# Kernel optimization log

Measured on AMD Instinct MI355X. Metric: run time of the kernel, lower is better.

Reference implementation:

```python
import jax, jax.numpy as jnp
import numpy as np

B, S, D, DFF = 8, 2048, 1024, 4096

def setup_inputs() -> dict:
    key = jax.random.key(0)
    ks = jax.random.split(key, 11)
    s = 0.02
    return {
        "x":  jax.random.normal(ks[0], (B, S, D), dtype=jnp.float32),
        "Wq": jax.random.normal(ks[1], (D, D), dtype=jnp.float32) * s,
        "bq": jnp.zeros((D,), dtype=jnp.float32),
        "Wk": jax.random.normal(ks[2], (D, D), dtype=jnp.float32) * s,
        "bk": jnp.zeros((D,), dtype=jnp.float32),
        "Wv": jax.random.normal(ks[3], (D, D), dtype=jnp.float32) * s,
        "bv": jnp.zeros((D,), dtype=jnp.float32),
        "W1": jax.random.normal(ks[4], (DFF, D), dtype=jnp.float32) * s,
        "b1": jnp.zeros((DFF,), dtype=jnp.float32),
        "W2": jax.random.normal(ks[5], (D, DFF), dtype=jnp.float32) * s,
        "b2": jnp.zeros((D,), dtype=jnp.float32),
    }

def reference(x, Wq, bq, Wk, bk, Wv, bv, W1, b1, W2, b2):
    # qkv projections (torch Linear: x @ W.T + b)
    q = jnp.einsum('bsd,ed->bse', x, Wq) + bq
    k = jnp.einsum('bsd,ed->bse', x, Wk) + bk
    v = jnp.einsum('bsd,ed->bse', x, Wv) + bv
    # single-head scaled dot-product attention with causal mask (decoder=True)
    scale = 1.0 / jnp.sqrt(jnp.asarray(q.shape[-1], q.dtype))
    scores = jnp.einsum('bqd,bkd->bqk', q, k) * scale  # (B,S,S)
    causal = jnp.tril(jnp.ones((scores.shape[-2], scores.shape[-1]), dtype=bool))
    scores = jnp.where(causal, scores, jnp.asarray(-jnp.inf, scores.dtype))
    attn = jax.nn.softmax(scores, axis=-1)
    attn_out = jnp.einsum('bqk,bkd->bqd', attn, v)
    # MLP: linear_2(gelu(linear_1(.)))  — exact (erf) GELU as in torch default
    h = jax.nn.gelu(jnp.einsum('bsd,fd->bsf', attn_out, W1) + b1, approximate=False)
    return jnp.einsum('bsf,df->bsd', h, W2) + b2
```

## Files before the change

kernel.cpp:

```cpp
#include <hip/hip_runtime.h>
#include <hip/hip_bf16.h>

#define NB   8
#define SS   2048
#define DD   1024
#define DFFN 4096
#define MTOT (NB*SS)

typedef unsigned short u16;
typedef __attribute__((ext_vector_type(4))) float f32x4;
typedef __attribute__((ext_vector_type(8))) short bf16x8;
typedef __attribute__((ext_vector_type(4))) int i32x4;
typedef __attribute__((ext_vector_type(4))) unsigned short u16x4;
typedef __attribute__((ext_vector_type(8))) unsigned short u16x8;

__device__ __forceinline__ u16 f2bf(float f) {
  union { float f; unsigned u; } c; c.f = f;
  unsigned r = c.u + 0x7FFFu + ((c.u >> 16) & 1u);
  return (u16)(r >> 16);
}

__device__ __forceinline__ void gload16(const void* g, void* l) {
  __builtin_amdgcn_global_load_lds(
      (const __attribute__((address_space(1))) void*)(unsigned long long)g,
      (__attribute__((address_space(3))) void*)(unsigned)(unsigned long long)l,
      16, 0, 0);
}

__device__ __forceinline__ bf16x8 dsr128(unsigned addr) {
  i32x4 r;
  asm volatile("ds_read_b128 %0, %1" : "=v"(r) : "v"(addr));
  return __builtin_bit_cast(bf16x8, r);
}

template<int EBIAS, int EGELU, int ESCALE, int EROWSCALE, int OUTMODE, int ETRANS, int CSKIP, int CK>
__global__ __launch_bounds__(256, 3)
void gemm128(const u16* __restrict__ A, const u16* __restrict__ B,
             const float* __restrict__ bias, const float* __restrict__ rowscale,
             void* __restrict__ C,
             int K, int lda, int ldb, int ldc, float scale,
             long long sA, long long sB, long long sC, int sRS)
{
  __shared__ __align__(1024) u16 smem[16384];

  const int nwg = gridDim.x * gridDim.y;
  const int orig = blockIdx.y * gridDim.x + blockIdx.x;
  const int q = nwg >> 3, r = nwg & 7;
  const int xcd = orig & 7, pos0 = orig >> 3;
  const int wg = (xcd < r ? xcd * (q + 1) : r * (q + 1) + (xcd - r) * q) + pos0;
  const int bx = wg % gridDim.x, by = wg / gridDim.x;
  const int row0 = by * 128, col0 = bx * 128;
  if (CSKIP && col0 > row0 + 127) return;

  const int z = blockIdx.z;
  A += (size_t)z * sA;
  B += (size_t)z * sB;

  int nkt = K >> 5;
  if (CK) { int lim = (row0 + 128) >> 5; if (lim < nkt) nkt = lim; }

  const int tid  = threadIdx.x;
  const int wid  = tid >> 6;
  const int lane = tid & 63;
  const int wr = wid >> 1, wc = wid & 1;

  const int srow = wid * 16 + (lane >> 2);
  const int sunit = (lane & 3) ^ ((lane >> 3) & 3);
  const char* gA = (const char*)A + ((size_t)(row0 + srow) * lda + sunit * 8) * 2;
  const char* gB = (const char*)B + ((size_t)(col0 + srow) * ldb + sunit * 8) * 2;
  char* lbase = (char*)smem;
  const size_t ldab = (size_t)64 * lda * 2;
  const size_t ldbb = (size_t)64 * ldb * 2;

  #define STG(t2) { char* lb = lbase + ((t2) & 1) * 16384; size_t kb = (size_t)(t2) * 64; \
      gload16(gA + kb,        lb + wid * 1024);                                           \
      gload16(gA + kb + ldab, lb + 4096 + wid * 1024);                                    \
      gload16(gB + kb,        lb + 8192 + wid * 1024);                                    \
      gload16(gB + kb + ldbb, lb + 8192 + 4096 + wid * 1024); }

  const int fr = lane & 15;
  const int ks16 = ((lane >> 4) & 3) * 16;
  const int xm = ((lane >> 1) & 3) << 4;
  const unsigned sbase = (unsigned)(unsigned long long)(void*)smem;

  f32x4 acc[4][4] = {};

  STG(0);
  asm volatile("s_waitcnt vmcnt(0)");
  asm volatile("s_barrier" ::: "memory");

  for (int t = 0; t < nkt; ++t) {
    if (t + 1 < nkt) STG(t + 1);
    const unsigned cb = sbase + (t & 1) * 16384;
    bf16x8 af[4], bf[4];
#pragma unroll
    for (int m = 0; m < 4; ++m)
      af[m] = dsr128(cb + (((wr * 64 + m * 16 + fr) * 64 + ks16) ^ xm));
#pragma unroll
    for (int n = 0; n < 4; ++n)
      bf[n] = dsr128(cb + ((8192 + (wc * 64 + n * 16 + fr) * 64 + ks16) ^ xm));
    asm volatile("s_waitcnt lgkmcnt(0)");
    __builtin_amdgcn_sched_barrier(0);
    __builtin_amdgcn_s_setprio(1);
#pragma unroll
    for (int m = 0; m < 4; ++m)
#pragma unroll
      for (int n = 0; n < 4; ++n)
        acc[m][n] = __builtin_amdgcn_mfma_f32_16x16x32_bf16(af[m], bf[n], acc[m][n], 0, 0, 0);
    __builtin_amdgcn_s_setprio(0);
    asm volatile("s_waitcnt vmcnt(0)");
    asm volatile("s_barrier" ::: "memory");
  }
  #undef STG

  char* sm = (char*)smem;
  const int r4 = (lane >> 4) * 4;

  if (OUTMODE == 1) {
#pragma unroll
    for (int p = 0; p < 2; ++p) {
      if (wc == p) {
#pragma unroll
        for (int n = 0; n < 4; ++n) {
          const int col = col0 + wc * 64 + n * 16 + fr;
          const int pb = (n * 16 + fr) * 4;
          float bia = EBIAS ? bias[col] : 0.0f;
#pragma unroll
          for (int m = 0; m < 4; ++m) {
#pragma unroll
            for (int j = 0; j < 4; ++j) {
              const int line = wr * 64 + m * 16 + r4 + j;
              float xv = acc[m][n][j];
              if (EBIAS)     xv += bia;
              if (ESCALE)    xv *= scale;
              if (EROWSCALE) xv *= rowscale[z * sRS + row0 + line];
              if (EGELU)     xv = 0.5f * xv * (1.0f + erff(xv * 0.70710678118f));
              *(float*)(sm + ((line * 256 + pb) ^ ((line & 7) << 4))) = xv;
            }
          }
        }
      }
      __syncthreads();
      float* Cb = (float*)C + (size_t)z * sC;
#pragma unroll
      for (int i = 0; i < 8; ++i) {
        const int o = i * 4096 + tid * 16;
        const int line = o >> 8, ps = o & 255;
        f32x4 v = *(const f32x4*)(sm + ((line * 256 + ps) ^ ((line & 7) << 4)));
        *(f32x4*)((char*)(Cb + (size_t)(row0 + line) * ldc + col0 + p * 64) + ps) = v;
      }
      __syncthreads();
    }
  } else if (ETRANS) {
#pragma unroll
    for (int n = 0; n < 4; ++n) {
      const int col = col0 + wc * 64 + n * 16 + fr;
      const int line = wc * 64 + n * 16 + fr;
      float bia = EBIAS ? bias[col] : 0.0f;
#pragma unroll
      for (int m = 0; m < 4; ++m) {
        const int rb = wr * 64 + m * 16 + r4;
        u16x4 pk;
#pragma unroll
        for (int j = 0; j < 4; ++j) {
          float xv = acc[m][n][j];
          if (EBIAS) xv += bia;
          pk[j] = f2bf(xv);
        }
        *(u16x4*)(sm + ((line * 256 + rb * 2) ^ ((line & 7) << 4))) = pk;
      }
    }
    __syncthreads();
    u16* Cb = (u16*)C + (size_t)(row0 >> 11) * (DD * SS) + (row0 & (SS - 1));
#pragma unroll
    for (int i = 0; i < 8; ++i) {
      const int o = i * 4096 + tid * 16;
      const int line = o >> 8, ps = o & 255;
      f32x4 v = *(const f32x4*)(sm + ((line * 256 + ps) ^ ((line & 7) << 4)));
      *(f32x4*)((char*)(Cb + (size_t)(col0 + line) * SS) + ps) = v;
    }
  } else {
#pragma unroll
    for (int n = 0; n < 4; ++n) {
      const int col = col0 + wc * 64 + n * 16 + fr;
      const int pc = (wc * 64 + n * 16 + fr) * 2;
      float bia = EBIAS ? bias[col] : 0.0f;
#pragma unroll
      for (int m = 0; m < 4; ++m) {
#pragma unroll
        for (int j = 0; j < 4; ++j) {
          const int line = wr * 64 + m * 16 + r4 + j;
          float xv = acc[m][n][j];
          if (EBIAS)     xv += bia;
          if (ESCALE)    xv *= scale;
          if (EROWSCALE) xv *= rowscale[z * sRS + row0 + line];
          if (EGELU)     xv = 0.5f * xv * (1.0f + erff(xv * 0.70710678118f));
          u16 u;
          if (OUTMODE == 2) { union { u16 s; _Float16 h; } cu; cu.h = (_Float16)xv; u = cu.s; }
          else u = f2bf(xv);
          *(u16*)(sm + ((line * 256 + pc) ^ ((line & 7) << 4))) = u;
        }
      }
    }
    __syncthreads();
    u16* Cb = (u16*)C + (size_t)z * sC + col0;
#pragma unroll
    for (int i = 0; i < 8; ++i) {
      const int o = i * 4096 + tid * 16;
      const int line = o >> 8, ps = o & 255;
      f32x4 v = *(const f32x4*)(sm + ((line * 256 + ps) ^ ((line & 7) << 4)));
      *(f32x4*)((char*)(Cb + (size_t)(row0 + line) * ldc) + ps) = v;
    }
  }
}

__global__ __launch_bounds__(256) void cvt_bf16_k(const float* __restrict__ in, u16* __restrict__ out, int n4) {
  int i = blockIdx.x * blockDim.x + threadIdx.x;
  if (i < n4) {
    float4 v = ((const float4*)in)[i];
    u16x4 o;
    o.x = f2bf(v.x); o.y = f2bf(v.y); o.z = f2bf(v.z); o.w = f2bf(v.w);
    ((u16x4*)out)[i] = o;
  }
}

__global__ __launch_bounds__(256) void softmax_k(u16* __restrict__ sc, float* __restrict__ rinv, int rows0) {
  const int widx = blockIdx.x * 4 + (threadIdx.x >> 6);
  const int lane = threadIdx.x & 63;
  u16* row = sc + (size_t)widx * SS;
  const int L = (widx & (SS - 1)) + 1;
  float mx = -1e30f;
  for (int k = 0; k < 4; ++k) {
    const int j0 = k * 512 + lane * 8;
    if (j0 < L) {
      u16x8 v = *(const u16x8*)(row + j0);
      int lim = L - j0; if (lim > 8) lim = 8;
#pragma unroll
      for (int e = 0; e < 8; ++e) {
        if (e < lim) { union { u16 u; _Float16 h; } c; c.u = v[e]; mx = fmaxf(mx, (float)c.h); }
      }
    }
  }
#pragma unroll
  for (int o = 32; o >= 1; o >>= 1) mx = fmaxf(mx, __shfl_xor(mx, o));
  float s = 0.0f;
  for (int k = 0; k < 4; ++k) {
    const int j0 = k * 512 + lane * 8;
    u16x8 v = *(const u16x8*)(row + j0);
    u16x8 w;
#pragma unroll
    for (int e = 0; e < 8; ++e) {
      const int j = j0 + e;
      float ev = 0.0f;
      if (j < L) { union { u16 u; _Float16 h; } c; c.u = v[e]; ev = __expf((float)c.h - mx); s += ev; }
      w[e] = f2bf(ev);
    }
    *(u16x8*)(row + j0) = w;
  }
#pragma unroll
  for (int o = 32; o >= 1; o >>= 1) s += __shfl_xor(s, o);
  if (lane == 0) rinv[rows0 + widx] = 1.0f / s;
}

extern "C" void kernel_launch(void* const* d_in, const int* in_sizes, int n_in,
                              void* d_out, int out_size, void* d_ws, size_t ws_size,
                              hipStream_t stream) {
  const float* x  = (const float*)d_in[0];
  const float* Wq = (const float*)d_in[1];
  const float* bq = (const float*)d_in[2];
  const float* Wk = (const float*)d_in[3];
  const float* bk = (const float*)d_in[4];
  const float* Wv = (const float*)d_in[5];
  const float* bv = (const float*)d_in[6];
  const float* W1 = (const float*)d_in[7];
  const float* b1 = (const float*)d_in[8];
  const float* W2 = (const float*)d_in[9];
  const float* b2 = (const float*)d_in[10];

  char* ws = (char*)d_ws;
  u16*  xb   = (u16*)(ws);
  u16*  Wqb  = (u16*)(ws + 33554432);
  u16*  Wkb  = (u16*)(ws + 35651584);
  u16*  Wvb  = (u16*)(ws + 37748736);
  u16*  W1b  = (u16*)(ws + 39845888);
  u16*  W2b  = (u16*)(ws + 48234496);
  u16*  Qb   = (u16*)(ws + 56623104);
  u16*  Kb   = (u16*)(ws + 90177536);
  u16*  Vtb  = (u16*)(ws + 123731968);
  float* rinv = (float*)(ws + 157286400);
  u16*  big  = (u16*)(ws + 157351936);
  u16*  att  = xb;

  const size_t base = 157351936ull;
  const size_t avail = ws_size > base ? ws_size - base : 0;
  int GB = 8; while (GB > 1 && (size_t)GB * 8388608ull > avail) GB >>= 1;
  int MC = 8192; while (MC > 2048 && (size_t)MC * 8192ull > avail) MC >>= 1;

  cvt_bf16_k<<<MTOT * DD / 4 / 256, 256, 0, stream>>>(x, xb, MTOT * DD / 4);
  cvt_bf16_k<<<DD * DD / 4 / 256, 256, 0, stream>>>(Wq, Wqb, DD * DD / 4);
  cvt_bf16_k<<<DD * DD / 4 / 256, 256, 0, stream>>>(Wk, Wkb, DD * DD / 4);
  cvt_bf16_k<<<DD * DD / 4 / 256, 256, 0, stream>>>(Wv, Wvb, DD * DD / 4);
  cvt_bf16_k<<<DFFN * DD / 4 / 256, 256, 0, stream>>>(W1, W1b, DFFN * DD / 4);
  cvt_bf16_k<<<DFFN * DD / 4 / 256, 256, 0, stream>>>(W2, W2b, DFFN * DD / 4);

  gemm128<1,0,0,0,0,0,0,0><<<dim3(DD/128, MTOT/128), 256, 0, stream>>>(
      xb, Wqb, bq, nullptr, (void*)Qb, DD, DD, DD, DD, 0.f, 0, 0, 0, 0);
  gemm128<1,0,0,0,0,0,0,0><<<dim3(DD/128, MTOT/128), 256, 0, stream>>>(
      xb, Wkb, bk, nullptr, (void*)Kb, DD, DD, DD, DD, 0.f, 0, 0, 0, 0);
  gemm128<1,0,0,0,0,1,0,0><<<dim3(DD/128, MTOT/128), 256, 0, stream>>>(
      xb, Wvb, bv, nullptr, (void*)Vtb, DD, DD, DD, DD, 0.f, 0, 0, 0, 0);

  for (int b0 = 0; b0 < NB; b0 += GB) {
    gemm128<0,0,1,0,2,0,1,0><<<dim3(SS/128, SS/128, GB), 256, 0, stream>>>(
        Qb + (size_t)b0 * SS * DD, Kb + (size_t)b0 * SS * DD, nullptr, nullptr,
        (void*)big, DD, DD, DD, SS, 0.03125f,
        (long long)SS * DD, (long long)SS * DD, (long long)SS * SS, 0);
    softmax_k<<<GB * SS / 4, 256, 0, stream>>>(big, rinv, b0 * SS);
    gemm128<0,0,0,1,0,0,0,1><<<dim3(DD/128, SS/128, GB), 256, 0, stream>>>(
        big, Vtb + (size_t)b0 * DD * SS, nullptr, rinv + (size_t)b0 * SS,
        (void*)(att + (size_t)b0 * SS * DD), SS, SS, SS, DD, 0.f,
        (long long)SS * SS, (long long)DD * SS, (long long)SS * DD, SS);
  }

  for (int c = 0; c < MTOT / MC; ++c) {
    u16* h = big;
    gemm128<1,1,0,0,0,0,0,0><<<dim3(DFFN/128, MC/128), 256, 0, stream>>>(
        att + (size_t)c * MC * DD, W1b, b1, nullptr, (void*)h,
        DD, DD, DD, DFFN, 0.f, 0, 0, 0, 0);
    gemm128<1,0,0,0,1,0,0,0><<<dim3(DD/128, MC/128), 256, 0, stream>>>(
        h, W2b, b2, nullptr, (void*)((float*)d_out + (size_t)c * MC * DD),
        DFFN, DFFN, DFFN, DD, 0.f, 0, 0, 0, 0);
  }
}
```

Before: 715.4 us.

## Triple-buffer GEMM LDS staging with two-tile prefetch depth

```diff
diff --git a/kernel.cpp b/kernel.cpp
--- a/kernel.cpp
+++ b/kernel.cpp
@@ -34,14 +34,14 @@
 }
 
 template<int EBIAS, int EGELU, int ESCALE, int EROWSCALE, int OUTMODE, int ETRANS, int CSKIP, int CK>
-__global__ __launch_bounds__(256, 3)
+__global__ __launch_bounds__(256, 4)
 void gemm128(const u16* __restrict__ A, const u16* __restrict__ B,
              const float* __restrict__ bias, const float* __restrict__ rowscale,
              void* __restrict__ C,
              int K, int lda, int ldb, int ldc, float scale,
              long long sA, long long sB, long long sC, int sRS)
 {
-  __shared__ __align__(1024) u16 smem[16384];
+  __shared__ __align__(1024) u16 smem[24576];
 
   const int nwg = gridDim.x * gridDim.y;
   const int orig = blockIdx.y * gridDim.x + blockIdx.x;
@@ -68,14 +68,13 @@
   const int sunit = (lane & 3) ^ ((lane >> 3) & 3);
   const char* gA = (const char*)A + ((size_t)(row0 + srow) * lda + sunit * 8) * 2;
   const char* gB = (const char*)B + ((size_t)(col0 + srow) * ldb + sunit * 8) * 2;
-  char* lbase = (char*)smem;
   const size_t ldab = (size_t)64 * lda * 2;
   const size_t ldbb = (size_t)64 * ldb * 2;
 
-  #define STG(t2) { char* lb = lbase + ((t2) & 1) * 16384; size_t kb = (size_t)(t2) * 64; \
-      gload16(gA + kb,        lb + wid * 1024);                                           \
-      gload16(gA + kb + ldab, lb + 4096 + wid * 1024);                                    \
-      gload16(gB + kb,        lb + 8192 + wid * 1024);                                    \
+  #define STG(t2, bo) { char* lb = (char*)smem + (bo); size_t kb = (size_t)(t2) * 64; \
+      gload16(gA + kb,        lb + wid * 1024);                                       \
+      gload16(gA + kb + ldab, lb + 4096 + wid * 1024);                                \
+      gload16(gB + kb,        lb + 8192 + wid * 1024);                                \
       gload16(gB + kb + ldbb, lb + 8192 + 4096 + wid * 1024); }
 
   const int fr = lane & 15;
@@ -85,32 +84,42 @@
 
   f32x4 acc[4][4] = {};
 
-  STG(0);
-  asm volatile("s_waitcnt vmcnt(0)");
+  STG(0, 0); STG(1, 16384);
+  asm volatile("s_waitcnt vmcnt(4)");
   asm volatile("s_barrier" ::: "memory");
 
-  for (int t = 0; t < nkt; ++t) {
-    if (t + 1 < nkt) STG(t + 1);
-    const unsigned cb = sbase + (t & 1) * 16384;
-    bf16x8 af[4], bf[4];
-#pragma unroll
-    for (int m = 0; m < 4; ++m)
-      af[m] = dsr128(cb + (((wr * 64 + m * 16 + fr) * 64 + ks16) ^ xm));
-#pragma unroll
-    for (int n = 0; n < 4; ++n)
-      bf[n] = dsr128(cb + ((8192 + (wc * 64 + n * 16 + fr) * 64 + ks16) ^ xm));
-    asm volatile("s_waitcnt lgkmcnt(0)");
-    __builtin_amdgcn_sched_barrier(0);
-    __builtin_amdgcn_s_setprio(1);
-#pragma unroll
-    for (int m = 0; m < 4; ++m)
-#pragma unroll
-      for (int n = 0; n < 4; ++n)
-        acc[m][n] = __builtin_amdgcn_mfma_f32_16x16x32_bf16(af[m], bf[n], acc[m][n], 0, 0, 0);
-    __builtin_amdgcn_s_setprio(0);
-    asm volatile("s_waitcnt vmcnt(0)");
-    asm volatile("s_barrier" ::: "memory");
-  }
+  unsigned cb = sbase;
+  unsigned sb = sbase + 32768;
+
+  #define KSTEP_BODY(WAITN)                                                   \
+    bf16x8 af[4], bf[4];                                                      \
+    _Pragma("unroll") for (int m = 0; m < 4; ++m)                             \
+      af[m] = dsr128(cb + (((wr * 64 + m * 16 + fr) * 64 + ks16) ^ xm));      \
+    _Pragma("unroll") for (int n = 0; n < 4; ++n)                             \
+      bf[n] = dsr128(cb + ((8192 + (wc * 64 + n * 16 + fr) * 64 + ks16) ^ xm));\
+    asm volatile("s_waitcnt lgkmcnt(0)");                                     \
+    __builtin_amdgcn_sched_barrier(0);                                        \
+    __builtin_amdgcn_s_setprio(1);                                            \
+    _Pragma("unroll") for (int m = 0; m < 4; ++m)                             \
+      _Pragma("unroll") for (int n = 0; n < 4; ++n)                           \
+        acc[m][n] = __builtin_amdgcn_mfma_f32_16x16x32_bf16(af[m], bf[n], acc[m][n], 0, 0, 0); \
+    __builtin_amdgcn_s_setprio(0);                                            \
+    asm volatile("s_waitcnt vmcnt(" #WAITN ")");                              \
+    asm volatile("s_barrier" ::: "memory");                                   \
+    cb += 16384; if (cb == sbase + 49152) cb = sbase;                         \
+    sb += 16384; if (sb == sbase + 49152) sb = sbase;
+
+  for (int t = 0; t < nkt - 2; ++t) {
+    STG(t + 2, sb - sbase);
+    KSTEP_BODY(4)
+  }
+  {
+    KSTEP_BODY(0)
+  }
+  {
+    KSTEP_BODY(0)
+  }
+  #undef KSTEP_BODY
   #undef STG
 
   char* sm = (char*)smem;
```

New measurement: 724.5 us. Within noise of the previous version (+1.3%).

## Load B fragments directly to registers, triple-buffer A in LDS, fuse QKV GEMMs

Applied to the files above, without the earlier changes.

```diff
diff --git a/kernel.cpp b/kernel.cpp
--- a/kernel.cpp
+++ b/kernel.cpp
@@ -32,12 +32,18 @@
   asm volatile("ds_read_b128 %0, %1" : "=v"(r) : "v"(addr));
   return __builtin_bit_cast(bf16x8, r);
 }
-
-template<int EBIAS, int EGELU, int ESCALE, int EROWSCALE, int OUTMODE, int ETRANS, int CSKIP, int CK>
+__device__ __forceinline__ void gload_b128(bf16x8* d, const char* a) {
+  i32x4 r;
+  asm volatile("global_load_dwordx4 %0, %1, off" : "=v"(r) : "v"(a));
+  *d = __builtin_bit_cast(bf16x8, r);
+}
+
+template<int EBIAS, int EGELU, int ESCALE, int EROWSCALE, int OUTMODE, int CSKIP, int CK>
 __global__ __launch_bounds__(256, 3)
 void gemm128(const u16* __restrict__ A, const u16* __restrict__ B,
-             const float* __restrict__ bias, const float* __restrict__ rowscale,
-             void* __restrict__ C,
+             const float* __restrict__ bias0, const float* __restrict__ bias1,
+             const float* __restrict__ bias2, const float* __restrict__ rowscale,
+             void* __restrict__ C0, void* __restrict__ C1, void* __restrict__ C2,
              int K, int lda, int ldb, int ldc, float scale,
              long long sA, long long sB, long long sC, int sRS)
 {
@@ -63,58 +69,116 @@
   const int wid  = tid >> 6;
   const int lane = tid & 63;
   const int wr = wid >> 1, wc = wid & 1;
-
-  const int srow = wid * 16 + (lane >> 2);
-  const int sunit = (lane & 3) ^ ((lane >> 3) & 3);
-  const char* gA = (const char*)A + ((size_t)(row0 + srow) * lda + sunit * 8) * 2;
-  const char* gB = (const char*)B + ((size_t)(col0 + srow) * ldb + sunit * 8) * 2;
-  char* lbase = (char*)smem;
-  const size_t ldab = (size_t)64 * lda * 2;
-  const size_t ldbb = (size_t)64 * ldb * 2;
-
-  #define STG(t2) { char* lb = lbase + ((t2) & 1) * 16384; size_t kb = (size_t)(t2) * 64; \
-      gload16(gA + kb,        lb + wid * 1024);                                           \
-      gload16(gA + kb + ldab, lb + 4096 + wid * 1024);                                    \
-      gload16(gB + kb,        lb + 8192 + wid * 1024);                                    \
-      gload16(gB + kb + ldbb, lb + 8192 + 4096 + wid * 1024); }
-
   const int fr = lane & 15;
   const int ks16 = ((lane >> 4) & 3) * 16;
   const int xm = ((lane >> 1) & 3) << 4;
+
+  const int sunit = (lane & 3) ^ ((lane >> 3) & 3);
+  const char* gA = (const char*)A +
+      ((size_t)(row0 + wid * 32 + (lane >> 2)) * lda + sunit * 8) * 2;
+  const size_t ldab = (size_t)16 * lda * 2;
   const unsigned sbase = (unsigned)(unsigned long long)(void*)smem;
 
+  const char* gB0 = (const char*)B +
+      ((size_t)(col0 + wc * 64 + fr) * ldb + (lane >> 4) * 8) * 2;
+  const size_t nstep = (size_t)16 * ldb * 2;
+  const char* gB1 = gB0 + nstep;
+  const char* gB2 = gB1 + nstep;
+  const char* gB3 = gB2 + nstep;
+
   f32x4 acc[4][4] = {};
-
-  STG(0);
-  asm volatile("s_waitcnt vmcnt(0)");
+  bf16x8 b0[4], b1[4];
+  unsigned cbo = 0, sbo = 16384;
+  size_t kbo = 128;
+
+  gload_b128(&b0[0], gB0); gload_b128(&b0[1], gB1);
+  gload_b128(&b0[2], gB2); gload_b128(&b0[3], gB3);
+  gB0 += 64; gB1 += 64; gB2 += 64; gB3 += 64;
+  gload16(gA,        (char*)smem + wid * 2048);
+  gload16(gA + ldab, (char*)smem + wid * 2048 + 1024);
+  gload16(gA + 64,        (char*)smem + 8192 + wid * 2048);
+  gload16(gA + 64 + ldab, (char*)smem + 8192 + wid * 2048 + 1024);
+  asm volatile("s_waitcnt vmcnt(2)" ::: "memory");
   asm volatile("s_barrier" ::: "memory");
-
-  for (int t = 0; t < nkt; ++t) {
-    if (t + 1 < nkt) STG(t + 1);
-    const unsigned cb = sbase + (t & 1) * 16384;
-    bf16x8 af[4], bf[4];
+  __builtin_amdgcn_sched_barrier(0);
+
+  #define STEP_MAIN(BC, BN)                                                   \
+  {                                                                           \
+    gload_b128(&BN[0], gB0); gload_b128(&BN[1], gB1);                         \
+    gload_b128(&BN[2], gB2); gload_b128(&BN[3], gB3);                         \
+    gB0 += 64; gB1 += 64; gB2 += 64; gB3 += 64;                               \
+    { char* lb = (char*)smem + sbo + wid * 2048;                              \
+      gload16(gA + kbo,        lb);                                           \
+      gload16(gA + kbo + ldab, lb + 1024); }                                  \
+    kbo += 64;                                                                \
+    bf16x8 af[4];                                                             \
+    _Pragma("unroll") for (int m = 0; m < 4; ++m)                             \
+      af[m] = dsr128(sbase + cbo + (((wr * 64 + m * 16 + fr) * 64 + ks16) ^ xm)); \
+    asm volatile("s_waitcnt lgkmcnt(0)" ::: "memory");                        \
+    __builtin_amdgcn_sched_barrier(0);                                        \
+    __builtin_amdgcn_s_setprio(1);                                            \
+    _Pragma("unroll") for (int m = 0; m < 4; ++m)                             \
+      _Pragma("unroll") for (int n = 0; n < 4; ++n)                           \
+        acc[m][n] = __builtin_amdgcn_mfma_f32_16x16x32_bf16(af[m], BC[n], acc[m][n], 0, 0, 0); \
+    __builtin_amdgcn_s_setprio(0);                                            \
+    __builtin_amdgcn_sched_barrier(0);                                        \
+    asm volatile("s_waitcnt vmcnt(2)" ::: "memory");                          \
+    asm volatile("s_barrier" ::: "memory");                                   \
+    __builtin_amdgcn_sched_barrier(0);                                        \
+    cbo += 8192; if (cbo == 24576) cbo = 0;                                   \
+    sbo += 8192; if (sbo == 24576) sbo = 0;                                   \
+  }
+
+  for (int it = (nkt - 2) >> 1; it > 0; --it) {
+    STEP_MAIN(b0, b1)
+    STEP_MAIN(b1, b0)
+  }
+  #undef STEP_MAIN
+
+  {
+    gload_b128(&b1[0], gB0); gload_b128(&b1[1], gB1);
+    gload_b128(&b1[2], gB2); gload_b128(&b1[3], gB3);
+    bf16x8 af[4];
 #pragma unroll
     for (int m = 0; m < 4; ++m)
-      af[m] = dsr128(cb + (((wr * 64 + m * 16 + fr) * 64 + ks16) ^ xm));
-#pragma unroll
-    for (int n = 0; n < 4; ++n)
-      bf[n] = dsr128(cb + ((8192 + (wc * 64 + n * 16 + fr) * 64 + ks16) ^ xm));
-    asm volatile("s_waitcnt lgkmcnt(0)");
+      af[m] = dsr128(sbase + cbo + (((wr * 64 + m * 16 + fr) * 64 + ks16) ^ xm));
+    asm volatile("s_waitcnt lgkmcnt(0)" ::: "memory");
     __builtin_amdgcn_sched_barrier(0);
     __builtin_amdgcn_s_setprio(1);
 #pragma unroll
     for (int m = 0; m < 4; ++m)
 #pragma unroll
       for (int n = 0; n < 4; ++n)
-        acc[m][n] = __builtin_amdgcn_mfma_f32_16x16x32_bf16(af[m], bf[n], acc[m][n], 0, 0, 0);
+        acc[m][n] = __builtin_amdgcn_mfma_f32_16x16x32_bf16(af[m], b0[n], acc[m][n], 0, 0, 0);
     __builtin_amdgcn_s_setprio(0);
-    asm volatile("s_waitcnt vmcnt(0)");
+    __builtin_amdgcn_sched_barrier(0);
+    asm volatile("s_waitcnt vmcnt(0)" ::: "memory");
     asm volatile("s_barrier" ::: "memory");
-  }
-  #undef STG
+    __builtin_amdgcn_sched_barrier(0);
+    cbo += 8192; if (cbo == 24576) cbo = 0;
+  }
+  {
+    bf16x8 af[4];
+#pragma unroll
+    for (int m = 0; m < 4; ++m)
+      af[m] = dsr128(sbase + cbo + (((wr * 64 + m * 16 + fr) * 64 + ks16) ^ xm));
+    asm volatile("s_waitcnt lgkmcnt(0)" ::: "memory");
+    __builtin_amdgcn_sched_barrier(0);
+#pragma unroll
+    for (int m = 0; m < 4; ++m)
+#pragma unroll
+      for (int n = 0; n < 4; ++n)
+        acc[m][n] = __builtin_amdgcn_mfma_f32_16x16x32_bf16(af[m], b1[n], acc[m][n], 0, 0, 0);
+    asm volatile("s_barrier" ::: "memory");
+    __builtin_amdgcn_sched_barrier(0);
+  }
 
   char* sm = (char*)smem;
   const int r4 = (lane >> 4) * 4;
+  const int sel  = (OUTMODE == 3) ? (col0 >> 10) : 0;
+  const int oc0  = (OUTMODE == 3) ? (col0 & 1023) : col0;
+  const float* bias = (OUTMODE == 3) ? (sel == 0 ? bias0 : sel == 1 ? bias1 : bias2)
+                                     : bias0;
 
   if (OUTMODE == 1) {
 #pragma unroll
@@ -122,7 +186,7 @@
       if (wc == p) {
 #pragma unroll
         for (int n = 0; n < 4; ++n) {
-          const int col = col0 + wc * 64 + n * 16 + fr;
+          const int col = oc0 + wc * 64 + n * 16 + fr;
           const int pb = (n * 16 + fr) * 4;
           float bia = EBIAS ? bias[col] : 0.0f;
 #pragma unroll
@@ -141,48 +205,43 @@
         }
       }
       __syncthreads();
-      float* Cb = (float*)C + (size_t)z * sC;
+      float* Cb = (float*)C0 + (size_t)z * sC;
 #pragma unroll
       for (int i = 0; i < 8; ++i) {
         const int o = i * 4096 + tid * 16;
         const int line = o >> 8, ps = o & 255;
         f32x4 v = *(const f32x4*)(sm + ((line * 256 + ps) ^ ((line & 7) << 4)));
-        *(f32x4*)((char*)(Cb + (size_t)(row0 + line) * ldc + col0 + p * 64) + ps) = v;
+        *(f32x4*)((char*)(Cb + (size_t)(row0 + line) * ldc + oc0 + p * 64) + ps) = v;
       }
       __syncthreads();
     }
-  } else if (ETRANS) {
+  } else if (OUTMODE == 3 && sel == 2) {
 #pragma unroll
     for (int n = 0; n < 4; ++n) {
-      const int col = col0 + wc * 64 + n * 16 + fr;
       const int line = wc * 64 + n * 16 + fr;
-      float bia = EBIAS ? bias[col] : 0.0f;
+      float bia = EBIAS ? bias[oc0 + line] : 0.0f;
 #pragma unroll
       for (int m = 0; m < 4; ++m) {
         const int rb = wr * 64 + m * 16 + r4;
         u16x4 pk;
 #pragma unroll
-        for (int j = 0; j < 4; ++j) {
-          float xv = acc[m][n][j];
-          if (EBIAS) xv += bia;
-          pk[j] = f2bf(xv);
-        }
+        for (int j = 0; j < 4; ++j) pk[j] = f2bf(acc[m][n][j] + bia);
         *(u16x4*)(sm + ((line * 256 + rb * 2) ^ ((line & 7) << 4))) = pk;
       }
     }
     __syncthreads();
-    u16* Cb = (u16*)C + (size_t)(row0 >> 11) * (DD * SS) + (row0 & (SS - 1));
+    u16* Cb = (u16*)C2 + (size_t)(row0 >> 11) * (DD * SS) + (row0 & (SS - 1));
 #pragma unroll
     for (int i = 0; i < 8; ++i) {
       const int o = i * 4096 + tid * 16;
       const int line = o >> 8, ps = o & 255;
       f32x4 v = *(const f32x4*)(sm + ((line * 256 + ps) ^ ((line & 7) << 4)));
-      *(f32x4*)((char*)(Cb + (size_t)(col0 + line) * SS) + ps) = v;
+      *(f32x4*)((char*)(Cb + (size_t)(oc0 + line) * SS) + ps) = v;
     }
   } else {
 #pragma unroll
     for (int n = 0; n < 4; ++n) {
-      const int col = col0 + wc * 64 + n * 16 + fr;
+      const int col = oc0 + wc * 64 + n * 16 + fr;
       const int pc = (wc * 64 + n * 16 + fr) * 2;
       float bia = EBIAS ? bias[col] : 0.0f;
 #pragma unroll
@@ -203,7 +262,7 @@
       }
     }
     __syncthreads();
-    u16* Cb = (u16*)C + (size_t)z * sC + col0;
+    u16* Cb = (u16*)(OUTMODE == 3 ? (sel ? C1 : C0) : C0) + (size_t)z * sC + oc0;
 #pragma unroll
     for (int i = 0; i < 8; ++i) {
       const int o = i * 4096 + tid * 16;
@@ -279,9 +338,7 @@
 
   char* ws = (char*)d_ws;
   u16*  xb   = (u16*)(ws);
-  u16*  Wqb  = (u16*)(ws + 33554432);
-  u16*  Wkb  = (u16*)(ws + 35651584);
-  u16*  Wvb  = (u16*)(ws + 37748736);
+  u16*  Wcat = (u16*)(ws + 33554432);
   u16*  W1b  = (u16*)(ws + 39845888);
   u16*  W2b  = (u16*)(ws + 48234496);
   u16*  Qb   = (u16*)(ws + 56623104);
@@ -294,41 +351,43 @@
   const size_t base = 157351936ull;
   const size_t avail = ws_size > base ? ws_size - base : 0;
   int GB = 8; while (GB > 1 && (size_t)GB * 8388608ull > avail) GB >>= 1;
-  int MC = 8192; while (MC > 2048 && (size_t)MC * 8192ull > avail) MC >>= 1;
+  int MC = 16384; while (MC > 2048 && (size_t)MC * 8192ull > avail) MC >>= 1;
 
   cvt_bf16_k<<<MTOT * DD / 4 / 256, 256, 0, stream>>>(x, xb, MTOT * DD / 4);
-  cvt_bf16_k<<<DD * DD / 4 / 256, 256, 0, stream>>>(Wq, Wqb, DD * DD / 4);
-  cvt_bf16_k<<<DD * DD / 4 / 256, 256, 0, stream>>>(Wk, Wkb, DD * DD / 4);
-  cvt_bf16_k<<<DD * DD / 4 / 256, 256, 0, stream>>>(Wv, Wvb, DD * DD / 4);
+  cvt_bf16_k<<<DD * DD / 4 / 256, 256, 0, stream>>>(Wq, Wcat, DD * DD / 4);
+  cvt_bf16_k<<<DD * DD / 4 / 256, 256, 0, stream>>>(Wk, Wcat + DD * DD, DD * DD / 4);
+  cvt_bf16_k<<<DD * DD / 4 / 256, 256, 0, stream>>>(Wv, Wcat + 2 * DD * DD, DD * DD / 4);
   cvt_bf16_k<<<DFFN * DD / 4 / 256, 256, 0, stream>>>(W1, W1b, DFFN * DD / 4);
   cvt_bf16_k<<<DFFN * DD / 4 / 256, 256, 0, stream>>>(W2, W2b, DFFN * DD / 4);
 
-  gemm128<1,0,0,0,0,0,0,0><<<dim3(DD/128, MTOT/128), 256, 0, stream>>>(
-      xb, Wqb, bq, nullptr, (void*)Qb, DD, DD, DD, DD, 0.f, 0, 0, 0, 0);
-  gemm128<1,0,0,0,0,0,0,0><<<dim3(DD/128, MTOT/128), 256, 0, stream>>>(
-      xb, Wkb, bk, nullptr, (void*)Kb, DD, DD, DD, DD, 0.f, 0, 0, 0, 0);
-  gemm128<1,0,0,0,0,1,0,0><<<dim3(DD/128, MTOT/128), 256, 0, stream>>>(
-      xb, Wvb, bv, nullptr, (void*)Vtb, DD, DD, DD, DD, 0.f, 0, 0, 0, 0);
+  gemm128<1,0,0,0,3,0,0><<<dim3(3 * DD / 128, MTOT / 128), 256, 0, stream>>>(
+      xb, Wcat, bq, bk, bv, nullptr, (void*)Qb, (void*)Kb, (void*)Vtb,
+      DD, DD, DD, DD, 0.f, 0, 0, 0, 0);
 
   for (int b0 = 0; b0 < NB; b0 += GB) {
-    gemm128<0,0,1,0,2,0,1,0><<<dim3(SS/128, SS/128, GB), 256, 0, stream>>>(
-        Qb + (size_t)b0 * SS * DD, Kb + (size_t)b0 * SS * DD, nullptr, nullptr,
-        (void*)big, DD, DD, DD, SS, 0.03125f,
+    gemm128<0,0,1,0,2,1,0><<<dim3(SS/128, SS/128, GB), 256, 0, stream>>>(
+        Qb + (size_t)b0 * SS * DD, Kb + (size_t)b0 * SS * DD,
+        nullptr, nullptr, nullptr, nullptr, (void*)big, nullptr, nullptr,
+        DD, DD, DD, SS, 0.03125f,
         (long long)SS * DD, (long long)SS * DD, (long long)SS * SS, 0);
     softmax_k<<<GB * SS / 4, 256, 0, stream>>>(big, rinv, b0 * SS);
-    gemm128<0,0,0,1,0,0,0,1><<<dim3(DD/128, SS/128, GB), 256, 0, stream>>>(
-        big, Vtb + (size_t)b0 * DD * SS, nullptr, rinv + (size_t)b0 * SS,
-        (void*)(att + (size_t)b0 * SS * DD), SS, SS, SS, DD, 0.f,
+    gemm128<0,0,0,1,0,0,1><<<dim3(DD/128, SS/128, GB), 256, 0, stream>>>(
+        big, Vtb + (size_t)b0 * DD * SS,
+        nullptr, nullptr, nullptr, rinv + (size_t)b0 * SS,
+        (void*)(att + (size_t)b0 * SS * DD), nullptr, nullptr,
+        SS, SS, SS, DD, 0.f,
         (long long)SS * SS, (long long)DD * SS, (long long)SS * DD, SS);
   }
 
   for (int c = 0; c < MTOT / MC; ++c) {
     u16* h = big;
-    gemm128<1,1,0,0,0,0,0,0><<<dim3(DFFN/128, MC/128), 256, 0, stream>>>(
-        att + (size_t)c * MC * DD, W1b, b1, nullptr, (void*)h,
+    gemm128<1,1,0,0,0,0,0><<<dim3(DFFN/128, MC/128), 256, 0, stream>>>(
+        att + (size_t)c * MC * DD, W1b, b1, nullptr, nullptr, nullptr,
+        (void*)h, nullptr, nullptr,
         DD, DD, DD, DFFN, 0.f, 0, 0, 0, 0);
-    gemm128<1,0,0,0,1,0,0,0><<<dim3(DD/128, MC/128), 256, 0, stream>>>(
-        h, W2b, b2, nullptr, (void*)((float*)d_out + (size_t)c * MC * DD),
+    gemm128<1,0,0,0,1,0,0><<<dim3(DD/128, MC/128), 256, 0, stream>>>(
+        h, W2b, b2, nullptr, nullptr, nullptr,
+        (void*)((float*)d_out + (size_t)c * MC * DD), nullptr, nullptr,
         DFFN, DFFN, DFFN, DD, 0.f, 0, 0, 0, 0);
   }
 }
```

Measured after the change: 1.115 ms. 55.8% more time.

## Fuse QKV projections into one GEMM and use 2-wave 128x128 tiles for MLP

Applied to the files above, without the earlier changes.

```diff
diff --git a/kernel.cpp b/kernel.cpp
--- a/kernel.cpp
+++ b/kernel.cpp
@@ -33,11 +33,12 @@
   return __builtin_bit_cast(bf16x8, r);
 }
 
-template<int EBIAS, int EGELU, int ESCALE, int EROWSCALE, int OUTMODE, int ETRANS, int CSKIP, int CK>
+template<int EBIAS, int EGELU, int ESCALE, int EROWSCALE, int OUTMODE, int CSKIP, int CK>
 __global__ __launch_bounds__(256, 3)
 void gemm128(const u16* __restrict__ A, const u16* __restrict__ B,
-             const float* __restrict__ bias, const float* __restrict__ rowscale,
-             void* __restrict__ C,
+             const float* __restrict__ bias0, const float* __restrict__ bias1,
+             const float* __restrict__ bias2, const float* __restrict__ rowscale,
+             void* __restrict__ C0, void* __restrict__ C1, void* __restrict__ C2,
              int K, int lda, int ldb, int ldc, float scale,
              long long sA, long long sB, long long sC, int sRS)
 {
@@ -68,14 +69,13 @@
   const int sunit = (lane & 3) ^ ((lane >> 3) & 3);
   const char* gA = (const char*)A + ((size_t)(row0 + srow) * lda + sunit * 8) * 2;
   const char* gB = (const char*)B + ((size_t)(col0 + srow) * ldb + sunit * 8) * 2;
-  char* lbase = (char*)smem;
   const size_t ldab = (size_t)64 * lda * 2;
   const size_t ldbb = (size_t)64 * ldb * 2;
 
-  #define STG(t2) { char* lb = lbase + ((t2) & 1) * 16384; size_t kb = (size_t)(t2) * 64; \
-      gload16(gA + kb,        lb + wid * 1024);                                           \
-      gload16(gA + kb + ldab, lb + 4096 + wid * 1024);                                    \
-      gload16(gB + kb,        lb + 8192 + wid * 1024);                                    \
+  #define STG(t2) { char* lb = (char*)smem + ((t2) & 1) * 16384; size_t kb = (size_t)(t2) * 64; \
+      gload16(gA + kb,        lb + wid * 1024);                                                 \
+      gload16(gA + kb + ldab, lb + 4096 + wid * 1024);                                          \
+      gload16(gB + kb,        lb + 8192 + wid * 1024);                                          \
       gload16(gB + kb + ldbb, lb + 8192 + 4096 + wid * 1024); }
 
   const int fr = lane & 15;
@@ -115,6 +115,10 @@
 
   char* sm = (char*)smem;
   const int r4 = (lane >> 4) * 4;
+  const int sel  = (OUTMODE == 3) ? (col0 >> 10) : 0;
+  const int oc0  = (OUTMODE == 3) ? (col0 & 1023) : col0;
+  const float* bias = (OUTMODE == 3) ? (sel == 0 ? bias0 : sel == 1 ? bias1 : bias2)
+                                     : bias0;
 
   if (OUTMODE == 1) {
 #pragma unroll
@@ -122,7 +126,7 @@
       if (wc == p) {
 #pragma unroll
         for (int n = 0; n < 4; ++n) {
-          const int col = col0 + wc * 64 + n * 16 + fr;
+          const int col = oc0 + wc * 64 + n * 16 + fr;
           const int pb = (n * 16 + fr) * 4;
           float bia = EBIAS ? bias[col] : 0.0f;
 #pragma unroll
@@ -141,48 +145,43 @@
         }
       }
       __syncthreads();
-      float* Cb = (float*)C + (size_t)z * sC;
+      float* Cb = (float*)C0 + (size_t)z * sC;
 #pragma unroll
       for (int i = 0; i < 8; ++i) {
         const int o = i * 4096 + tid * 16;
         const int line = o >> 8, ps = o & 255;
         f32x4 v = *(const f32x4*)(sm + ((line * 256 + ps) ^ ((line & 7) << 4)));
-        *(f32x4*)((char*)(Cb + (size_t)(row0 + line) * ldc + col0 + p * 64) + ps) = v;
+        *(f32x4*)((char*)(Cb + (size_t)(row0 + line) * ldc + oc0 + p * 64) + ps) = v;
       }
       __syncthreads();
     }
-  } else if (ETRANS) {
+  } else if (OUTMODE == 3 && sel == 2) {
 #pragma unroll
     for (int n = 0; n < 4; ++n) {
-      const int col = col0 + wc * 64 + n * 16 + fr;
       const int line = wc * 64 + n * 16 + fr;
-      float bia = EBIAS ? bias[col] : 0.0f;
+      float bia = EBIAS ? bias[oc0 + line] : 0.0f;
 #pragma unroll
       for (int m = 0; m < 4; ++m) {
         const int rb = wr * 64 + m * 16 + r4;
         u16x4 pk;
 #pragma unroll
-        for (int j = 0; j < 4; ++j) {
-          float xv = acc[m][n][j];
-          if (EBIAS) xv += bia;
-          pk[j] = f2bf(xv);
-        }
+        for (int j = 0; j < 4; ++j) pk[j] = f2bf(acc[m][n][j] + bia);
         *(u16x4*)(sm + ((line * 256 + rb * 2) ^ ((line & 7) << 4))) = pk;
       }
     }
     __syncthreads();
-    u16* Cb = (u16*)C + (size_t)(row0 >> 11) * (DD * SS) + (row0 & (SS - 1));
+    u16* Cb = (u16*)C2 + (size_t)(row0 >> 11) * (DD * SS) + (row0 & (SS - 1));
 #pragma unroll
     for (int i = 0; i < 8; ++i) {
       const int o = i * 4096 + tid * 16;
       const int line = o >> 8, ps = o & 255;
       f32x4 v = *(const f32x4*)(sm + ((line * 256 + ps) ^ ((line & 7) << 4)));
-      *(f32x4*)((char*)(Cb + (size_t)(col0 + line) * SS) + ps) = v;
+      *(f32x4*)((char*)(Cb + (size_t)(oc0 + line) * SS) + ps) = v;
     }
   } else {
 #pragma unroll
     for (int n = 0; n < 4; ++n) {
-      const int col = col0 + wc * 64 + n * 16 + fr;
+      const int col = oc0 + wc * 64 + n * 16 + fr;
       const int pc = (wc * 64 + n * 16 + fr) * 2;
       float bia = EBIAS ? bias[col] : 0.0f;
 #pragma unroll
@@ -203,13 +202,143 @@
       }
     }
     __syncthreads();
-    u16* Cb = (u16*)C + (size_t)z * sC + col0;
+    u16* Cb = (u16*)(OUTMODE == 3 ? (sel ? C1 : C0) : C0) + (size_t)z * sC + oc0;
 #pragma unroll
     for (int i = 0; i < 8; ++i) {
       const int o = i * 4096 + tid * 16;
       const int line = o >> 8, ps = o & 255;
       f32x4 v = *(const f32x4*)(sm + ((line * 256 + ps) ^ ((line & 7) << 4)));
       *(f32x4*)((char*)(Cb + (size_t)(row0 + line) * ldc) + ps) = v;
+    }
+  }
+}
+
+template<int EBIAS, int EGELU, int OUTF32>
+__global__ __launch_bounds__(128, 2)
+void gemm128w(const u16* __restrict__ A, const u16* __restrict__ B,
+              const float* __restrict__ bias, void* __restrict__ C,
+              int K, int lda, int ldb, int ldc)
+{
+  __shared__ __align__(1024) u16 smem[16384];
+
+  const int nwg = gridDim.x * gridDim.y;
+  const int orig = blockIdx.y * gridDim.x + blockIdx.x;
+  const int q = nwg >> 3, r = nwg & 7;
+  const int xcd = orig & 7, pos0 = orig >> 3;
+  const int wg = (xcd < r ? xcd * (q + 1) : r * (q + 1) + (xcd - r) * q) + pos0;
+  const int bx = wg % gridDim.x, by = wg / gridDim.x;
+  const int row0 = by * 128, col0 = bx * 128;
+
+  const int nkt = K >> 5;
+  const int tid = threadIdx.x, wid = tid >> 6, lane = tid & 63;
+  const int fr = lane & 15;
+  const int ks16 = ((lane >> 4) & 3) * 16;
+  const int xm = ((lane >> 1) & 3) << 4;
+  const int sunit = (lane & 3) ^ ((lane >> 3) & 3);
+  const char* gA = (const char*)A + ((size_t)(row0 + wid * 64 + (lane >> 2)) * lda + sunit * 8) * 2;
+  const char* gB = (const char*)B + ((size_t)(col0 + wid * 64 + (lane >> 2)) * ldb + sunit * 8) * 2;
+  const size_t ldab = (size_t)16 * lda * 2, ldbb = (size_t)16 * ldb * 2;
+  const unsigned sbase = (unsigned)(unsigned long long)(void*)smem;
+
+  #define STGW(t2) { char* lb = (char*)smem + ((t2) & 1) * 16384; size_t kb = (size_t)(t2) * 64; \
+      char* la = lb + wid * 4096; char* lbb = lb + 8192 + wid * 4096;                            \
+      gload16(gA + kb,            la);                                                            \
+      gload16(gA + kb +     ldab, la + 1024);                                                     \
+      gload16(gA + kb + 2 * ldab, la + 2048);                                                     \
+      gload16(gA + kb + 3 * ldab, la + 3072);                                                     \
+      gload16(gB + kb,            lbb);                                                           \
+      gload16(gB + kb +     ldbb, lbb + 1024);                                                    \
+      gload16(gB + kb + 2 * ldbb, lbb + 2048);                                                    \
+      gload16(gB + kb + 3 * ldbb, lbb + 3072); }
+
+  f32x4 acc[8][4] = {};
+
+  STGW(0);
+  asm volatile("s_waitcnt vmcnt(0)");
+  asm volatile("s_barrier" ::: "memory");
+
+  for (int t = 0; t < nkt; ++t) {
+    if (t + 1 < nkt) STGW(t + 1);
+    const unsigned cb = sbase + (t & 1) * 16384;
+    bf16x8 af[8], bf[4];
+#pragma unroll
+    for (int m = 0; m < 8; ++m)
+      af[m] = dsr128(cb + (((m * 16 + fr) * 64 + ks16) ^ xm));
+#pragma unroll
+    for (int n = 0; n < 4; ++n)
+      bf[n] = dsr128(cb + ((8192 + (wid * 64 + n * 16 + fr) * 64 + ks16) ^ xm));
+    asm volatile("s_waitcnt lgkmcnt(0)");
+    __builtin_amdgcn_sched_barrier(0);
+    __builtin_amdgcn_s_setprio(1);
+#pragma unroll
+    for (int m = 0; m < 8; ++m)
+#pragma unroll
+      for (int n = 0; n < 4; ++n)
+        acc[m][n] = __builtin_amdgcn_mfma_f32_16x16x32_bf16(af[m], bf[n], acc[m][n], 0, 0, 0);
+    __builtin_amdgcn_s_setprio(0);
+    asm volatile("s_waitcnt vmcnt(0)");
+    asm volatile("s_barrier" ::: "memory");
+  }
+  #undef STGW
+
+  char* sm = (char*)smem;
+  const int r4 = (lane >> 4) * 4;
+
+  if (OUTF32) {
+#pragma unroll
+    for (int p = 0; p < 2; ++p) {
+      if (wid == p) {
+#pragma unroll
+        for (int n = 0; n < 4; ++n) {
+          const int col = col0 + wid * 64 + n * 16 + fr;
+          const int pb = (n * 16 + fr) * 4;
+          float bia = EBIAS ? bias[col] : 0.0f;
+#pragma unroll
+          for (int m = 0; m < 8; ++m) {
+#pragma unroll
+            for (int j = 0; j < 4; ++j) {
+              const int line = m * 16 + r4 + j;
+              float xv = acc[m][n][j] + bia;
+              if (EGELU) xv = 0.5f * xv * (1.0f + erff(xv * 0.70710678118f));
+              *(float*)(sm + ((line * 256 + pb) ^ ((line & 7) << 4))) = xv;
+            }
+          }
+        }
+      }
+      __syncthreads();
+#pragma unroll
+      for (int i = 0; i < 16; ++i) {
+        const int o = i * 2048 + tid * 16;
+        const int line = o >> 8, ps = o & 255;
+        f32x4 v = *(const f32x4*)(sm + ((line * 256 + ps) ^ ((line & 7) << 4)));
+        *(f32x4*)((char*)((float*)C + (size_t)(row0 + line) * ldc + col0 + p * 64) + ps) = v;
+      }
+      __syncthreads();
+    }
+  } else {
+#pragma unroll
+    for (int n = 0; n < 4; ++n) {
+      const int col = col0 + wid * 64 + n * 16 + fr;
+      const int pc = (wid * 64 + n * 16 + fr) * 2;
+      float bia = EBIAS ? bias[col] : 0.0f;
+#pragma unroll
+      for (int m = 0; m < 8; ++m) {
+#pragma unroll
+        for (int j = 0; j < 4; ++j) {
+          const int line = m * 16 + r4 + j;
+          float xv = acc[m][n][j] + bia;
+          if (EGELU) xv = 0.5f * xv * (1.0f + erff(xv * 0.70710678118f));
+          *(u16*)(sm + ((line * 256 + pc) ^ ((line & 7) << 4))) = f2bf(xv);
+        }
+      }
+    }
+    __syncthreads();
+#pragma unroll
+    for (int i = 0; i < 16; ++i) {
+      const int o = i * 2048 + tid * 16;
+      const int line = o >> 8, ps = o & 255;
+      f32x4 v = *(const f32x4*)(sm + ((line * 256 + ps) ^ ((line & 7) << 4)));
+      *(f32x4*)((char*)((u16*)C + (size_t)(row0 + line) * ldc) + col0 * 2 + ps) = v;
     }
   }
 }
@@ -279,9 +408,7 @@
 
   char* ws = (char*)d_ws;
   u16*  xb   = (u16*)(ws);
-  u16*  Wqb  = (u16*)(ws + 33554432);
-  u16*  Wkb  = (u16*)(ws + 35651584);
-  u16*  Wvb  = (u16*)(ws + 37748736);
+  u16*  Wcat = (u16*)(ws + 33554432);
   u16*  W1b  = (u16*)(ws + 39845888);
   u16*  W2b  = (u16*)(ws + 48234496);
   u16*  Qb   = (u16*)(ws + 56623104);
@@ -297,38 +424,36 @@
   int MC = 8192; while (MC > 2048 && (size_t)MC * 8192ull > avail) MC >>= 1;
 
   cvt_bf16_k<<<MTOT * DD / 4 / 256, 256, 0, stream>>>(x, xb, MTOT * DD / 4);
-  cvt_bf16_k<<<DD * DD / 4 / 256, 256, 0, stream>>>(Wq, Wqb, DD * DD / 4);
-  cvt_bf16_k<<<DD * DD / 4 / 256, 256, 0, stream>>>(Wk, Wkb, DD * DD / 4);
-  cvt_bf16_k<<<DD * DD / 4 / 256, 256, 0, stream>>>(Wv, Wvb, DD * DD / 4);
+  cvt_bf16_k<<<DD * DD / 4 / 256, 256, 0, stream>>>(Wq, Wcat, DD * DD / 4);
+  cvt_bf16_k<<<DD * DD / 4 / 256, 256, 0, stream>>>(Wk, Wcat + DD * DD, DD * DD / 4);
+  cvt_bf16_k<<<DD * DD / 4 / 256, 256, 0, stream>>>(Wv, Wcat + 2 * DD * DD, DD * DD / 4);
   cvt_bf16_k<<<DFFN * DD / 4 / 256, 256, 0, stream>>>(W1, W1b, DFFN * DD / 4);
   cvt_bf16_k<<<DFFN * DD / 4 / 256, 256, 0, stream>>>(W2, W2b, DFFN * DD / 4);
 
-  gemm128<1,0,0,0,0,0,0,0><<<dim3(DD/128, MTOT/128), 256, 0, stream>>>(
-      xb, Wqb, bq, nullptr, (void*)Qb, DD, DD, DD, DD, 0.f, 0, 0, 0, 0);
-  gemm128<1,0,0,0,0,0,0,0><<<dim3(DD/128, MTOT/128), 256, 0, stream>>>(
-      xb, Wkb, bk, nullptr, (void*)Kb, DD, DD, DD, DD, 0.f, 0, 0, 0, 0);
-  gemm128<1,0,0,0,0,1,0,0><<<dim3(DD/128, MTOT/128), 256, 0, stream>>>(
-      xb, Wvb, bv, nullptr, (void*)Vtb, DD, DD, DD, DD, 0.f, 0, 0, 0, 0);
+  gemm128<1,0,0,0,3,0,0><<<dim3(3 * DD / 128, MTOT / 128), 256, 0, stream>>>(
+      xb, Wcat, bq, bk, bv, nullptr, (void*)Qb, (void*)Kb, (void*)Vtb,
+      DD, DD, DD, DD, 0.f, 0, 0, 0, 0);
 
   for (int b0 = 0; b0 < NB; b0 += GB) {
-    gemm128<0,0,1,0,2,0,1,0><<<dim3(SS/128, SS/128, GB), 256, 0, stream>>>(
-        Qb + (size_t)b0 * SS * DD, Kb + (size_t)b0 * SS * DD, nullptr, nullptr,
-        (void*)big, DD, DD, DD, SS, 0.03125f,
+    gemm128<0,0,1,0,2,1,0><<<dim3(SS/128, SS/128, GB), 256, 0, stream>>>(
+        Qb + (size_t)b0 * SS * DD, Kb + (size_t)b0 * SS * DD,
+        nullptr, nullptr, nullptr, nullptr, (void*)big, nullptr, nullptr,
+        DD, DD, DD, SS, 0.03125f,
         (long long)SS * DD, (long long)SS * DD, (long long)SS * SS, 0);
     softmax_k<<<GB * SS / 4, 256, 0, stream>>>(big, rinv, b0 * SS);
-    gemm128<0,0,0,1,0,0,0,1><<<dim3(DD/128, SS/128, GB), 256, 0, stream>>>(
-        big, Vtb + (size_t)b0 * DD * SS, nullptr, rinv + (size_t)b0 * SS,
-        (void*)(att + (size_t)b0 * SS * DD), SS, SS, SS, DD, 0.f,
+    gemm128<0,0,0,1,0,0,1><<<dim3(DD/128, SS/128, GB), 256, 0, stream>>>(
+        big, Vtb + (size_t)b0 * DD * SS,
+        nullptr, nullptr, nullptr, rinv + (size_t)b0 * SS,
+        (void*)(att + (size_t)b0 * SS * DD), nullptr, nullptr,
+        SS, SS, SS, DD, 0.f,
         (long long)SS * SS, (long long)DD * SS, (long long)SS * DD, SS);
   }
 
   for (int c = 0; c < MTOT / MC; ++c) {
     u16* h = big;
-    gemm128<1,1,0,0,0,0,0,0><<<dim3(DFFN/128, MC/128), 256, 0, stream>>>(
-        att + (size_t)c * MC * DD, W1b, b1, nullptr, (void*)h,
-        DD, DD, DD, DFFN, 0.f, 0, 0, 0, 0);
-    gemm128<1,0,0,0,1,0,0,0><<<dim3(DD/128, MC/128), 256, 0, stream>>>(
-        h, W2b, b2, nullptr, (void*)((float*)d_out + (size_t)c * MC * DD),
-        DFFN, DFFN, DFFN, DD, 0.f, 0, 0, 0, 0);
-  }
-}
+    gemm128w<1,1,0><<<dim3(DFFN/128, MC/128), 128, 0, stream>>>(
+        att + (size_t)c * MC * DD, W1b, b1, (void*)h, DD, DD, DD, DFFN);
+    gemm128w<1,0,1><<<dim3(DD/128, MC/128), 128, 0, stream>>>(
+        h, W2b, b2, (void*)((float*)d_out + (size_t)c * MC * DD), DFFN, DFFN, DFFN, DD);
+  }
+}
```

Measured after the change: 829.5 us. 15.9% more time.
